# Kernel optimization log

Hardware: AMD Instinct MI355X
Metric: run time of the kernel (lower is better)

## Reference

```python
import jax, jax.numpy as jnp
import numpy as np

NUM_NODES = 12288
NUM_GRAPHS = 1024
LEADS_PER_GRAPH = 12
SIG_LEN = 2048
NUM_EDGES = 196608


def _conv1d(x, w, b, stride, pad):
    # x: [N, C_in, L], w: [C_out, C_in, K]
    y = jax.lax.conv_general_dilated(
        x, w, window_strides=(stride,), padding=[(pad, pad)],
        dimension_numbers=("NCH", "OIH", "NCH"))
    return y + b[None, :, None]


def _gcn(x, src, dst, W, b, n_nodes):
    # PyG GCNConv: add self-loops, symmetric deg^-1/2 normalization.
    h = x @ W  # [N, out]
    loop = jnp.arange(n_nodes, dtype=src.dtype)
    s = jnp.concatenate([src, loop])
    d = jnp.concatenate([dst, loop])
    deg = jax.ops.segment_sum(jnp.ones(d.shape, h.dtype), d, num_segments=n_nodes)
    dis = jax.lax.rsqrt(deg)  # deg >= 1 due to self-loops
    norm = dis[s] * dis[d]  # [E+N]
    return jax.ops.segment_sum(h[s] * norm[:, None], d, num_segments=n_nodes) + b


def setup_inputs() -> dict:
    key = jax.random.key(0)
    ks = jax.random.split(key, 16)
    f = jnp.float32
    inp = {
        "x_raw": jax.random.normal(ks[0], (NUM_NODES, SIG_LEN), f),
        "conv1_w": jax.random.normal(ks[1], (16, 1, 7), f) * 0.2,
        "conv1_b": jax.random.normal(ks[2], (16,), f) * 0.05,
        "conv2_w": jax.random.normal(ks[3], (32, 16, 5), f) * 0.1,
        "conv2_b": jax.random.normal(ks[4], (32,), f) * 0.05,
        "lin_w": jax.random.normal(ks[5], (32, 64), f) * 0.15,
        "lin_b": jax.random.normal(ks[6], (64,), f) * 0.05,
        "gnn1_w": jax.random.normal(ks[7], (64, 128), f) * 0.1,
        "gnn1_b": jax.random.normal(ks[8], (128,), f) * 0.05,
        "gnn2_w": jax.random.normal(ks[9], (128, 128), f) * 0.08,
        "gnn2_b": jax.random.normal(ks[10], (128,), f) * 0.05,
        "fc_w": jax.random.normal(ks[11], (128, 5), f) * 0.08,
        "fc_b": jax.random.normal(ks[12], (5,), f) * 0.05,
        "edge_index": jax.random.randint(ks[13], (2, NUM_EDGES), 0, NUM_NODES, jnp.int32),
        "batch": (jnp.arange(NUM_NODES, dtype=jnp.int32) // LEADS_PER_GRAPH),
        "num_graphs": NUM_GRAPHS,
    }
    return inp


def reference(x_raw, conv1_w, conv1_b, conv2_w, conv2_b, lin_w, lin_b,
              gnn1_w, gnn1_b, gnn2_w, gnn2_b, fc_w, fc_b,
              edge_index, batch, num_graphs):
    n_nodes = x_raw.shape[0]
    # LeadCNN encoder
    h = x_raw[:, None, :]                              # [N,1,L]
    h = jax.nn.relu(_conv1d(h, conv1_w, conv1_b, 2, 3))  # [N,16,L/2]
    h = jax.nn.relu(_conv1d(h, conv2_w, conv2_b, 2, 2))  # [N,32,L/4]
    h = jnp.mean(h, axis=-1)                           # AdaptiveAvgPool1d(1)
    h = h @ lin_w + lin_b                              # [N,cnn_out]
    # Two GCN layers with ReLU
    src, dst = edge_index[0], edge_index[1]
    h = jax.nn.relu(_gcn(h, src, dst, gnn1_w, gnn1_b, n_nodes))
    h = jax.nn.relu(_gcn(h, src, dst, gnn2_w, gnn2_b, n_nodes))
    # global_mean_pool over batch
    sums = jax.ops.segment_sum(h, batch, num_segments=num_graphs)
    cnts = jax.ops.segment_sum(jnp.ones((n_nodes,), h.dtype), batch, num_segments=num_graphs)
    pooled = sums / jnp.maximum(cnts, 1.0)[:, None]
    return pooled @ fc_w + fc_b
```

## Files before the change

### kernel.cpp

```cpp
#include <hip/hip_runtime.h>
#include <cstddef>

#define N_NODES 12288
#define SIG     2048
#define C1N     16
#define L1N     1024
#define C2N     32
#define F0      64
#define F1      128
#define NEDGE   196608
#define NGRAPH  1024

typedef float    f32x4 __attribute__((ext_vector_type(4)));
typedef _Float16 f16x8 __attribute__((ext_vector_type(8)));
typedef __fp16   fp16x2_raw __attribute__((ext_vector_type(2)));

__device__ __forceinline__ unsigned pkrtz(float a, float b) {
    union { fp16x2_raw h; unsigned u; } c;
    c.h = __builtin_amdgcn_cvt_pkrtz(a, b);
    return c.u;
}

__global__ __launch_bounds__(256) void k_encoder(
    const float* __restrict__ x_raw,
    const float* __restrict__ conv1_w, const float* __restrict__ conv1_b,
    const float* __restrict__ conv2_w, const float* __restrict__ conv2_b,
    const float* __restrict__ lin_w,   const float* __restrict__ lin_b,
    float* __restrict__ h0)
{
    __shared__ __align__(16) unsigned xw[1056];
    __shared__ __align__(16) unsigned c1t[4 * 800];
    __shared__ float wmsum[4][C2N];
    __shared__ float mean_s[C2N];

    const int tid  = threadIdx.x;
    const int node = blockIdx.x;
    const int lane = tid & 63;
    const int wq   = tid >> 6;
    const int colL = lane & 15;
    const int hi8  = lane >> 4;
    const float* xrow = x_raw + (size_t)node * SIG;

    #pragma unroll
    for (int ii = 0; ii < 2; ++ii) {
        int i = lane + 64 * ii;
        if (i < 72) {
            int xb = 512 * wq + 8 * i - 8;
            float v[8];
            if (xb >= 0 && xb + 8 <= SIG) {
                float4 xa = *(const float4*)(xrow + xb);
                float4 xc = *(const float4*)(xrow + xb + 4);
                v[0] = xa.x; v[1] = xa.y; v[2] = xa.z; v[3] = xa.w;
                v[4] = xc.x; v[5] = xc.y; v[6] = xc.z; v[7] = xc.w;
            } else {
                #pragma unroll
                for (int t = 0; t < 8; ++t) {
                    int xi = xb + t;
                    v[t] = ((unsigned)xi < (unsigned)SIG) ? xrow[xi] : 0.f;
                }
            }
            uint4 w4;
            w4.x = pkrtz(v[0], v[1]); w4.y = pkrtz(v[2], v[3]);
            w4.z = pkrtz(v[4], v[5]); w4.w = pkrtz(v[6], v[7]);
            *(uint4*)&xw[256 * wq + 4 * i] = w4;
        }
    }

    f16x8 w1A;
    #pragma unroll
    for (int j = 0; j < 8; ++j) w1A[j] = (_Float16)0.f;
    if (hi8 == 0) {
        #pragma unroll
        for (int j = 1; j < 8; ++j) w1A[j] = (_Float16)conv1_w[colL * 7 + (j - 1)];
    }
    float bias1[4];
    #pragma unroll
    for (int r = 0; r < 4; ++r) bias1[r] = conv1_b[hi8 * 4 + r];

    f16x8 wA[2][3];
    #pragma unroll
    for (int mt = 0; mt < 2; ++mt) {
        const int oc = mt * 16 + colL;
        #pragma unroll
        for (int kt = 0; kt < 3; ++kt) {
            #pragma unroll
            for (int j = 0; j < 8; ++j) {
                const int ic  = 4 * hi8 + (j & 3);
                const int tap = 2 * kt + (j >> 2);
                wA[mt][kt][j] = (_Float16)((tap < 5) ? conv2_w[oc * 80 + ic * 5 + tap] : 0.f);
            }
        }
    }
    float bias2[2][4];
    #pragma unroll
    for (int mt = 0; mt < 2; ++mt)
        #pragma unroll
        for (int r = 0; r < 4; ++r)
            bias2[mt][r] = conv2_b[mt * 16 + hi8 * 4 + r];

    float msumr[2][4];
    #pragma unroll
    for (int mt = 0; mt < 2; ++mt)
        #pragma unroll
        for (int r = 0; r < 4; ++r) msumr[mt][r] = 0.f;

    unsigned* cw = &c1t[wq * 800];
    const int rb = 20 * colL + 2 * hi8;

    #pragma unroll 1
    for (int sp = 0; sp < 4; ++sp) {
        const int xwb = 256 * wq + 64 * sp;

        #pragma unroll
        for (int T = 0; T < 5; ++T) {
            const int wbase = xwb + 16 * T + colL + 4 * hi8;
            union { unsigned u[4]; f16x8 v; } Bx;
            #pragma unroll
            for (int u = 0; u < 4; ++u) Bx.u[u] = xw[wbase + u];
            f32x4 a;
            a[0] = bias1[0]; a[1] = bias1[1]; a[2] = bias1[2]; a[3] = bias1[3];
            a = __builtin_amdgcn_mfma_f32_16x16x32_f16(w1A, Bx.v, a, 0, 0, 0);
            uint2 wr;
            wr.x = pkrtz(fmaxf(a[0], 0.f), fmaxf(a[1], 0.f));
            wr.y = pkrtz(fmaxf(a[2], 0.f), fmaxf(a[3], 0.f));
            *(uint2*)&cw[(16 * T + colL) * 10 + 2 * hi8] = wr;
        }
        if (wq == 0 && sp == 0) {
            if (lane < 20) cw[lane] = 0u;
        }
        if (wq == 3 && sp == 3) {
            for (int k2 = lane; k2 < 140; k2 += 64) cw[660 + k2] = 0u;
        }

        #pragma unroll
        for (int nt = 0; nt < 2; ++nt) {
            f32x4 acc[2];
            #pragma unroll
            for (int mt = 0; mt < 2; ++mt) {
                acc[mt][0] = bias2[mt][0]; acc[mt][1] = bias2[mt][1];
                acc[mt][2] = bias2[mt][2]; acc[mt][3] = bias2[mt][3];
            }
            #pragma unroll
            for (int kt = 0; kt < 3; ++kt) {
                union { uint2 u[2]; f16x8 v; } B;
                B.u[0] = *(const uint2*)&cw[rb + 320 * nt + 20 * kt];
                B.u[1] = *(const uint2*)&cw[rb + 320 * nt + 20 * kt + 10];
                #pragma unroll
                for (int mt = 0; mt < 2; ++mt)
                    acc[mt] = __builtin_amdgcn_mfma_f32_16x16x32_f16(wA[mt][kt], B.v, acc[mt], 0, 0, 0);
            }
            #pragma unroll
            for (int mt = 0; mt < 2; ++mt)
                #pragma unroll
                for (int r = 0; r < 4; ++r)
                    msumr[mt][r] += fmaxf(acc[mt][r], 0.f);
        }
    }

    #pragma unroll
    for (int mt = 0; mt < 2; ++mt)
        #pragma unroll
        for (int r = 0; r < 4; ++r) {
            float s = msumr[mt][r];
            s += __shfl_xor(s, 1);
            s += __shfl_xor(s, 2);
            s += __shfl_xor(s, 4);
            s += __shfl_xor(s, 8);
            msumr[mt][r] = s;
        }
    if (colL == 0) {
        #pragma unroll
        for (int mt = 0; mt < 2; ++mt)
            #pragma unroll
            for (int r = 0; r < 4; ++r)
                wmsum[wq][mt * 16 + hi8 * 4 + r] = msumr[mt][r];
    }
    __syncthreads();

    if (tid < C2N) {
        float s = wmsum[0][tid] + wmsum[1][tid] + wmsum[2][tid] + wmsum[3][tid];
        mean_s[tid] = s * (1.f / 512.f);
    }
    __syncthreads();

    if (tid < F0) {
        float a = lin_b[tid];
        #pragma unroll
        for (int ic = 0; ic < C2N; ++ic)
            a = fmaf(mean_s[ic], lin_w[ic * F0 + tid], a);
        h0[(size_t)node * F0 + tid] = a;
    }
}

__global__ __launch_bounds__(256) void k_count_cnt(const int* __restrict__ dst,
                                                   const int* __restrict__ batch,
                                                   int* __restrict__ deg,
                                                   float* __restrict__ cnt)
{
    const int bid = blockIdx.x;
    if (bid < NEDGE / 256) {
        int e = bid * 256 + threadIdx.x;
        atomicAdd(&deg[dst[e]], 1);
    } else {
        int n = (bid - NEDGE / 256) * 256 + threadIdx.x;
        atomicAdd(&cnt[batch[n]], 1.f);
    }
}

__global__ __launch_bounds__(1024) void k_scan(const int* __restrict__ deg,
                                               int* __restrict__ rowptr,
                                               int* __restrict__ cursor,
                                               float* __restrict__ dis,
                                               float* __restrict__ invd)
{
    __shared__ int wtot[16];
    const int t = threadIdx.x;
    const int lane = t & 63, wvid = t >> 6;
    int d[12]; int s = 0;
    #pragma unroll
    for (int m = 0; m < 12; ++m) { d[m] = deg[12 * t + m]; s += d[m]; }
    const int mysum = s;
    #pragma unroll
    for (int off = 1; off < 64; off <<= 1) {
        int u = __shfl_up(s, off);
        if (lane >= off) s += u;
    }
    if (lane == 63) wtot[wvid] = s;
    __syncthreads();
    if (t < 16) {
        int v = wtot[t];
        #pragma unroll
        for (int off = 1; off < 16; off <<= 1) {
            int u = __shfl_up(v, off);
            if (t >= off) v += u;
        }
        wtot[t] = v;
    }
    __syncthreads();
    int run = (wvid ? wtot[wvid - 1] : 0) + (s - mysum);
    if (t == 0) rowptr[0] = 0;
    #pragma unroll
    for (int m = 0; m < 12; ++m) {
        const int i = 12 * t + m;
        cursor[i] = run;
        run += d[m];
        rowptr[i + 1] = run;
        float df = (float)(d[m] + 1);
        dis[i]  = rsqrtf(df);
        invd[i] = 1.f / df;
    }
}

__global__ __launch_bounds__(256) void k_scatter(const int* __restrict__ src,
                                                 const int* __restrict__ dst,
                                                 int* __restrict__ cursor,
                                                 int* __restrict__ csr)
{
    int e = blockIdx.x * 256 + threadIdx.x;
    if (e < NEDGE) {
        int d = dst[e];
        int idx = atomicAdd(&cursor[d], 1);
        csr[idx] = src[e];
    }
}

template <int K, int POOL>
__global__ __launch_bounds__(256) void k_gcn(
    const float* __restrict__ h, const int* __restrict__ rowptr,
    const int* __restrict__ csr, const float* __restrict__ dis,
    const float* __restrict__ invd, const float* __restrict__ W,
    const float* __restrict__ bvec, float* __restrict__ out,
    const int* __restrict__ batch, float* __restrict__ pooled)
{
    __shared__ float hs[8][K];
    const int tid = threadIdx.x;
    const int n0  = blockIdx.x * 8;

    const int npb = 256 / K;
    const int f   = tid & (K - 1);
    const int sub = tid / K;
    #pragma unroll
    for (int it = 0; it < 8 / npb; ++it) {
        const int nl = it * npb + sub;
        const int n  = n0 + nl;
        const float dn = dis[n];
        float a0 = h[(size_t)n * K + f] * invd[n];
        float a1 = 0.f, a2 = 0.f, a3 = 0.f;
        int e = rowptr[n];
        const int e1 = rowptr[n + 1];
        for (; e + 3 < e1; e += 4) {
            int s0 = csr[e], s1 = csr[e + 1], s2 = csr[e + 2], s3 = csr[e + 3];
            a0 = fmaf(h[(size_t)s0 * K + f], dis[s0] * dn, a0);
            a1 = fmaf(h[(size_t)s1 * K + f], dis[s1] * dn, a1);
            a2 = fmaf(h[(size_t)s2 * K + f], dis[s2] * dn, a2);
            a3 = fmaf(h[(size_t)s3 * K + f], dis[s3] * dn, a3);
        }
        for (; e < e1; ++e) {
            int s0 = csr[e];
            a0 = fmaf(h[(size_t)s0 * K + f], dis[s0] * dn, a0);
        }
        hs[nl][f] = (a0 + a1) + (a2 + a3);
    }
    __syncthreads();

    const int j    = tid & 127;
    const int half = tid >> 7;
    float a[4];
    #pragma unroll
    for (int c = 0; c < 4; ++c) a[c] = bvec[j];

    for (int k4 = 0; k4 < K; k4 += 4) {
        float w0 = W[(k4 + 0) * F1 + j];
        float w1 = W[(k4 + 1) * F1 + j];
        float w2 = W[(k4 + 2) * F1 + j];
        float w3 = W[(k4 + 3) * F1 + j];
        #pragma unroll
        for (int c = 0; c < 4; ++c) {
            float4 hv = *(const float4*)&hs[half * 4 + c][k4];
            a[c] = fmaf(hv.x, w0, a[c]);
            a[c] = fmaf(hv.y, w1, a[c]);
            a[c] = fmaf(hv.z, w2, a[c]);
            a[c] = fmaf(hv.w, w3, a[c]);
        }
    }
    #pragma unroll
    for (int c = 0; c < 4; ++c) {
        float r = fmaxf(a[c], 0.f);
        int n = n0 + half * 4 + c;
        if (POOL) atomicAdd(&pooled[(size_t)batch[n] * F1 + j], r);
        else      out[(size_t)n * F1 + j] = r;
    }
}

__global__ __launch_bounds__(128) void k_final(const float* __restrict__ pooled,
                                               const float* __restrict__ cnt,
                                               const float* __restrict__ fc_w,
                                               const float* __restrict__ fc_b,
                                               float* __restrict__ out)
{
    __shared__ float ps[F1];
    const int g = blockIdx.x, tid = threadIdx.x;
    float inv = 1.f / fmaxf(cnt[g], 1.f);
    ps[tid] = pooled[g * F1 + tid] * inv;
    __syncthreads();
    if (tid < 5) {
        float a = fc_b[tid];
        for (int f = 0; f < F1; ++f) a = fmaf(ps[f], fc_w[f * 5 + tid], a);
        out[g * 5 + tid] = a;
    }
}

extern "C" void kernel_launch(void* const* d_in, const int* in_sizes, int n_in,
                              void* d_out, int out_size, void* d_ws, size_t ws_size,
                              hipStream_t stream)
{
    const float* x_raw = (const float*)d_in[0];
    const float* c1w   = (const float*)d_in[1];
    const float* c1b   = (const float*)d_in[2];
    const float* c2w   = (const float*)d_in[3];
    const float* c2b   = (const float*)d_in[4];
    const float* lw    = (const float*)d_in[5];
    const float* lb    = (const float*)d_in[6];
    const float* g1w   = (const float*)d_in[7];
    const float* g1b   = (const float*)d_in[8];
    const float* g2w   = (const float*)d_in[9];
    const float* g2b   = (const float*)d_in[10];
    const float* fcw   = (const float*)d_in[11];
    const float* fcb   = (const float*)d_in[12];
    const int*   ei    = (const int*)d_in[13];
    const int*   batch = (const int*)d_in[14];
    const int* src = ei;
    const int* dst = ei + NEDGE;

    float* ws = (float*)d_ws;
    float* h0     = ws + 0;
    float* h1     = ws + 786432;
    float* dis    = ws + 2359296;
    float* invd   = ws + 2371584;
    float* pooled = ws + 2383872;
    float* cnt    = ws + 2514944;
    int*   deg    = (int*)(ws + 2515968);
    int*   rowptr = (int*)(ws + 2528256);
    int*   cursor = (int*)(ws + 2540548);
    int*   csr    = (int*)(ws + 2552836);

    float* out = (float*)d_out;

    hipMemsetAsync(deg, 0, N_NODES * sizeof(int), stream);
    hipMemsetAsync(pooled, 0, (size_t)(NGRAPH * F1 + NGRAPH) * sizeof(float), stream);

    k_encoder<<<N_NODES, 256, 0, stream>>>(x_raw, c1w, c1b, c2w, c2b, lw, lb, h0);
    k_count_cnt<<<NEDGE / 256 + N_NODES / 256, 256, 0, stream>>>(dst, batch, deg, cnt);
    k_scan<<<1, 1024, 0, stream>>>(deg, rowptr, cursor, dis, invd);
    k_scatter<<<NEDGE / 256, 256, 0, stream>>>(src, dst, cursor, csr);

    k_gcn<F0, 0><<<N_NODES / 8, 256, 0, stream>>>(h0, rowptr, csr, dis, invd, g1w, g1b, h1, batch, pooled);
    k_gcn<F1, 1><<<N_NODES / 8, 256, 0, stream>>>(h1, rowptr, csr, dis, invd, g2w, g2b, nullptr, batch, pooled);

    k_final<<<NGRAPH, 128, 0, stream>>>(pooled, cnt, fcw, fcb, out);
}
```

Baseline: 182.3 us.

## Process two nodes per encoder block and fold degree counting into encoder launch

The encoder now assigns two nodes per 256-thread block, with each pair of waves covering half of one node's signal, so each wave runs 8 segment iterations instead of 4 and the grid is half as large. The separate degree/count atomic kernel is folded into the encoder launch as extra trailing blocks, which removes one kernel launch and lets those atomics overlap with encoder work. The cost is a larger shared input buffer and longer per-wave work, which may change occupancy, and the atomic blocks are scheduled after the encoder blocks in the grid.

```diff
diff --git a/kernel.cpp b/kernel.cpp
--- a/kernel.cpp
+++ b/kernel.cpp
@@ -11,6 +11,9 @@
 #define NEDGE   196608
 #define NGRAPH  1024
 
+#define NB_ENC   (N_NODES / 2)
+#define CNT_BLKS (NEDGE / 256 + N_NODES / 256)
+
 typedef float    f32x4 __attribute__((ext_vector_type(4)));
 typedef _Float16 f16x8 __attribute__((ext_vector_type(8)));
 typedef __fp16   fp16x2_raw __attribute__((ext_vector_type(2)));
@@ -26,26 +29,43 @@
     const float* __restrict__ conv1_w, const float* __restrict__ conv1_b,
     const float* __restrict__ conv2_w, const float* __restrict__ conv2_b,
     const float* __restrict__ lin_w,   const float* __restrict__ lin_b,
-    float* __restrict__ h0)
-{
-    __shared__ __align__(16) unsigned xw[1056];
+    float* __restrict__ h0,
+    const int* __restrict__ dst, const int* __restrict__ batch,
+    int* __restrict__ deg, float* __restrict__ cnt)
+{
+    __shared__ __align__(16) unsigned xw[2][1056];
     __shared__ __align__(16) unsigned c1t[4 * 800];
     __shared__ float wmsum[4][C2N];
-    __shared__ float mean_s[C2N];
-
-    const int tid  = threadIdx.x;
-    const int node = blockIdx.x;
+    __shared__ float mean_s[2][C2N];
+
+    const int tid = threadIdx.x;
+
+    if (blockIdx.x >= NB_ENC) {
+        const int b = blockIdx.x - NB_ENC;
+        if (b < NEDGE / 256) {
+            atomicAdd(&deg[dst[b * 256 + tid]], 1);
+        } else {
+            atomicAdd(&cnt[batch[(b - NEDGE / 256) * 256 + tid]], 1.f);
+        }
+        return;
+    }
+
     const int lane = tid & 63;
     const int wq   = tid >> 6;
     const int colL = lane & 15;
     const int hi8  = lane >> 4;
+    const int ndl  = wq >> 1;
+    const int hf   = wq & 1;
+    const int node = blockIdx.x * 2 + ndl;
     const float* xrow = x_raw + (size_t)node * SIG;
-
-    #pragma unroll
-    for (int ii = 0; ii < 2; ++ii) {
-        int i = lane + 64 * ii;
-        if (i < 72) {
-            int xb = 512 * wq + 8 * i - 8;
+    unsigned* xn = &xw[ndl][0];
+
+    const int nqu = hf ? 132 : 136;
+    #pragma unroll
+    for (int it = 0; it < 3; ++it) {
+        int i = lane + 64 * it;
+        if (i < nqu) {
+            int xb = 1024 * hf + 8 * i - 8;
             float v[8];
             if (xb >= 0 && xb + 8 <= SIG) {
                 float4 xa = *(const float4*)(xrow + xb);
@@ -62,9 +82,10 @@
             uint4 w4;
             w4.x = pkrtz(v[0], v[1]); w4.y = pkrtz(v[2], v[3]);
             w4.z = pkrtz(v[4], v[5]); w4.w = pkrtz(v[6], v[7]);
-            *(uint4*)&xw[256 * wq + 4 * i] = w4;
-        }
-    }
+            *(uint4*)&xn[512 * hf + 4 * i] = w4;
+        }
+    }
+    if (hf == 1 && lane < 16) xn[1040 + lane] = 0u;
 
     f16x8 w1A;
     #pragma unroll
@@ -108,15 +129,15 @@
     const int rb = 20 * colL + 2 * hi8;
 
     #pragma unroll 1
-    for (int sp = 0; sp < 4; ++sp) {
-        const int xwb = 256 * wq + 64 * sp;
+    for (int sp = 0; sp < 8; ++sp) {
+        const int xwb = 512 * hf + 64 * sp;
 
         #pragma unroll
         for (int T = 0; T < 5; ++T) {
             const int wbase = xwb + 16 * T + colL + 4 * hi8;
             union { unsigned u[4]; f16x8 v; } Bx;
             #pragma unroll
-            for (int u = 0; u < 4; ++u) Bx.u[u] = xw[wbase + u];
+            for (int u = 0; u < 4; ++u) Bx.u[u] = xn[wbase + u];
             f32x4 a;
             a[0] = bias1[0]; a[1] = bias1[1]; a[2] = bias1[2]; a[3] = bias1[3];
             a = __builtin_amdgcn_mfma_f32_16x16x32_f16(w1A, Bx.v, a, 0, 0, 0);
@@ -125,10 +146,10 @@
             wr.y = pkrtz(fmaxf(a[2], 0.f), fmaxf(a[3], 0.f));
             *(uint2*)&cw[(16 * T + colL) * 10 + 2 * hi8] = wr;
         }
-        if (wq == 0 && sp == 0) {
+        if (hf == 0 && sp == 0) {
             if (lane < 20) cw[lane] = 0u;
         }
-        if (wq == 3 && sp == 3) {
+        if (hf == 1 && sp == 7) {
             for (int k2 = lane; k2 < 140; k2 += 64) cw[660 + k2] = 0u;
         }
 
@@ -177,33 +198,20 @@
     }
     __syncthreads();
 
-    if (tid < C2N) {
-        float s = wmsum[0][tid] + wmsum[1][tid] + wmsum[2][tid] + wmsum[3][tid];
-        mean_s[tid] = s * (1.f / 512.f);
-    }
-    __syncthreads();
-
-    if (tid < F0) {
-        float a = lin_b[tid];
+    if (tid < 64) {
+        const int nd2 = tid >> 5, oc = tid & 31;
+        mean_s[nd2][oc] = (wmsum[2 * nd2][oc] + wmsum[2 * nd2 + 1][oc]) * (1.f / 512.f);
+    }
+    __syncthreads();
+
+    if (tid < 128) {
+        const int nd2 = tid >> 6, o = tid & 63;
+        const int nodew = blockIdx.x * 2 + nd2;
+        float a = lin_b[o];
         #pragma unroll
         for (int ic = 0; ic < C2N; ++ic)
-            a = fmaf(mean_s[ic], lin_w[ic * F0 + tid], a);
-        h0[(size_t)node * F0 + tid] = a;
-    }
-}
-
-__global__ __launch_bounds__(256) void k_count_cnt(const int* __restrict__ dst,
-                                                   const int* __restrict__ batch,
-                                                   int* __restrict__ deg,
-                                                   float* __restrict__ cnt)
-{
-    const int bid = blockIdx.x;
-    if (bid < NEDGE / 256) {
-        int e = bid * 256 + threadIdx.x;
-        atomicAdd(&deg[dst[e]], 1);
-    } else {
-        int n = (bid - NEDGE / 256) * 256 + threadIdx.x;
-        atomicAdd(&cnt[batch[n]], 1.f);
+            a = fmaf(mean_s[nd2][ic], lin_w[ic * F0 + o], a);
+        h0[(size_t)nodew * F0 + o] = a;
     }
 }
 
@@ -389,8 +397,8 @@
     hipMemsetAsync(deg, 0, N_NODES * sizeof(int), stream);
     hipMemsetAsync(pooled, 0, (size_t)(NGRAPH * F1 + NGRAPH) * sizeof(float), stream);
 
-    k_encoder<<<N_NODES, 256, 0, stream>>>(x_raw, c1w, c1b, c2w, c2b, lw, lb, h0);
-    k_count_cnt<<<NEDGE / 256 + N_NODES / 256, 256, 0, stream>>>(dst, batch, deg, cnt);
+    k_encoder<<<NB_ENC + CNT_BLKS, 256, 0, stream>>>(
+        x_raw, c1w, c1b, c2w, c2b, lw, lb, h0, dst, batch, deg, cnt);
     k_scan<<<1, 1024, 0, stream>>>(deg, rowptr, cursor, dis, invd);
     k_scatter<<<NEDGE / 256, 256, 0, stream>>>(src, dst, cursor, csr);
 
```

After: 161.4 us. -11.5%, faster.
